# Kernel optimization log

Hardware: AMD Instinct MI355X
Metric: run time of the kernel (lower is better)

The kernel has to match this reference:

```python
import math
import jax, jax.numpy as jnp
import numpy as np

D = 128
R = 64
BETA = 1.0


def setup_inputs() -> dict:
    key = jax.random.key(0)
    k1, k2 = jax.random.split(key)
    X_tilde = jax.random.normal(k1, (8, 2048, D), dtype=jnp.float32)
    W = jax.random.normal(k2, (D, R), dtype=jnp.float32) / math.sqrt(R)
    return {"X_tilde": X_tilde, "W": W}


def reference(X_tilde, W):
    # S = W W^T / sqrt(d*r), shape (d, d)
    d, r = W.shape
    S = (W @ W.T) / math.sqrt(d * r)
    B, T, _ = X_tilde.shape
    # gram = X S X^T, shape (B, T, T)
    XS = jnp.einsum('btd,de->bte', X_tilde, S)
    gram = jnp.einsum('bte,bse->bts', XS, X_tilde)
    # trace-centering: subtract (tr(gram)/T) * I
    trace = jnp.einsum('btt->b', gram)  # (B,)
    eye = jnp.eye(T, dtype=X_tilde.dtype)
    centered = gram - (trace / T)[:, None, None] * eye[None, :, :]
    scores = centered / math.sqrt(d)  # normalize_sqrt_d=True
    A = jax.nn.softmax(BETA * scores, axis=-1)  # (B, T, T)
    Y_hat = jnp.einsum('bts,bsd->btd', A, X_tilde)
    return Y_hat
```

## Files before the change

kernel.cpp:

```cpp
#include <hip/hip_runtime.h>
#include <hip/hip_bf16.h>
#include <math.h>

#define D_DIM 128
#define R_DIM 64
#define T_DIM 2048
#define B_DIM 8
#define NS 4
#define SCHUNK (T_DIM / NS)
#define SBLK 32
#define NIT (SCHUNK / SBLK)
#define KE_CONST (0.08838834764831845f * 1.4426950408889634f)

typedef __attribute__((ext_vector_type(8))) short bf16x8;
typedef __attribute__((ext_vector_type(4))) short s16x4;
typedef __attribute__((ext_vector_type(4))) float f32x4;

__device__ inline unsigned short f2bf(float f) {
  union { float f; unsigned int u; } v; v.f = f;
  return (unsigned short)((v.u + 0x7FFFu + ((v.u >> 16) & 1u)) >> 16);
}
__device__ inline float bf2f(unsigned short u) {
  union { unsigned int u; float f; } v; v.u = ((unsigned int)u) << 16;
  return v.f;
}
__device__ inline unsigned int cvt_pk_bf16(float lo, float hi) {
  unsigned int r;
  asm("v_cvt_pk_bf16_f32 %0, %1, %2" : "=v"(r) : "v"(lo), "v"(hi));
  return r;
}

__device__ inline void async16(const short* l, const unsigned short* g) {
  __builtin_amdgcn_global_load_lds(
      (const __attribute__((address_space(1))) unsigned int*)g,
      (__attribute__((address_space(3))) unsigned int*)l, 16, 0, 0);
}

__global__ void k_s(const float* __restrict__ W, unsigned short* __restrict__ Sb) {
  int gid = blockIdx.x * 256 + threadIdx.x;
  int i = gid >> 7, j = gid & 127;
  const float* wi = W + i * R_DIM;
  const float* wj = W + j * R_DIM;
  float acc = 0.f;
#pragma unroll 8
  for (int r = 0; r < R_DIM; ++r) acc += wi[r] * wj[r];
  Sb[gid] = f2bf(acc * 0.011048543456039806f);
}

__global__ void __launch_bounds__(128) k_prep(
    const float* __restrict__ X, const unsigned short* __restrict__ Sb,
    unsigned short* __restrict__ Qb, unsigned short* __restrict__ Xb,
    unsigned short* __restrict__ Xt, float* __restrict__ part) {
  const int tid = threadIdx.x;
  const int w = tid >> 6, lane = tid & 63;
  const int g = lane >> 4, c = lane & 15;
  const int b = blockIdx.y;
  const int t0 = blockIdx.x * 32;
  const int tw = t0 + w * 16;

  __shared__ __align__(16) short xbT[D_DIM * 32];
  __shared__ float red[2];

  union FU { unsigned int wd[4]; bf16x8 v; };
  bf16x8 xf[4];
#pragma unroll
  for (int kc = 0; kc < 4; ++kc) {
    const float* xp = X + ((size_t)(b * T_DIM + tw + c)) * D_DIM + kc * 32 + g * 8;
    f32x4 a = *(const f32x4*)xp;
    f32x4 bb = *(const f32x4*)(xp + 4);
    FU f;
    f.wd[0] = cvt_pk_bf16(a[0], a[1]);
    f.wd[1] = cvt_pk_bf16(a[2], a[3]);
    f.wd[2] = cvt_pk_bf16(bb[0], bb[1]);
    f.wd[3] = cvt_pk_bf16(bb[2], bb[3]);
    xf[kc] = f.v;
    *(bf16x8*)(Xb + ((size_t)(b * T_DIM + tw + c)) * D_DIM + kc * 32 + g * 8) = f.v;
#pragma unroll
    for (int jw = 0; jw < 4; ++jw) {
      unsigned int wv = f.wd[jw];
      int e = kc * 32 + g * 8 + jw * 2;
      xbT[(e + 0) * 32 + w * 16 + c] = (short)wv;
      xbT[(e + 1) * 32 + w * 16 + c] = (short)(wv >> 16);
    }
  }

  f32x4 acc[8];
#pragma unroll
  for (int dc = 0; dc < 8; ++dc) acc[dc] = (f32x4){0.f, 0.f, 0.f, 0.f};
#pragma unroll
  for (int dc = 0; dc < 8; ++dc) {
    bf16x8 sf[4];
#pragma unroll
    for (int kc = 0; kc < 4; ++kc)
      sf[kc] = *(const bf16x8*)(Sb + (size_t)(dc * 16 + c) * D_DIM + kc * 32 + g * 8);
#pragma unroll
    for (int kc = 0; kc < 4; ++kc)
      acc[dc] = __builtin_amdgcn_mfma_f32_16x16x32_bf16(xf[kc], sf[kc], acc[dc], 0, 0, 0);
  }

  __syncthreads();

  float trp = 0.f;
#pragma unroll
  for (int dc = 0; dc < 8; ++dc)
#pragma unroll
    for (int r = 0; r < 4; ++r) {
      float q = acc[dc][r];
      float x = bf2f((unsigned short)xbT[(dc * 16 + c) * 32 + w * 16 + g * 4 + r]);
      trp += q * x;
      unsigned int pk = cvt_pk_bf16(q * KE_CONST, 0.f);
      Qb[((size_t)(b * T_DIM + tw + g * 4 + r)) * D_DIM + dc * 16 + c] = (unsigned short)pk;
    }

#pragma unroll
  for (int p = 0; p < 4; ++p) {
    int row = p * 32 + (tid >> 2);
    bf16x8 v = *(const bf16x8*)&xbT[row * 32 + (tid & 3) * 8];
    *(bf16x8*)(Xt + ((size_t)(b * D_DIM + row)) * T_DIM + t0 + (tid & 3) * 8) = v;
  }

  trp += __shfl_xor(trp, 1); trp += __shfl_xor(trp, 2);
  trp += __shfl_xor(trp, 4); trp += __shfl_xor(trp, 8);
  trp += __shfl_xor(trp, 16); trp += __shfl_xor(trp, 32);
  if (lane == 0) red[w] = trp;
  __syncthreads();
  if (tid == 0) part[b * 64 + blockIdx.x] = red[0] + red[1];
}

__global__ void __launch_bounds__(256, 2) k_attn(
    const unsigned short* __restrict__ Qb, const unsigned short* __restrict__ Xb,
    const unsigned short* __restrict__ Xt, const float* __restrict__ part,
    unsigned short* __restrict__ accp, float* __restrict__ rsp) {
  const int tid = threadIdx.x;
  const int wave = tid >> 6, lane = tid & 63;
  const int g = lane >> 4, c = lane & 15;
  const int lin = blockIdx.x;
  const int b = lin & 7;
  const int kk = lin >> 3;
  const int ns = kk & 3;
  const int t0w = (kk >> 2) * 128 + wave * 32;

  const unsigned short* Qbb = Qb + (size_t)b * T_DIM * D_DIM;
  const unsigned short* Xbb = Xb + (size_t)b * T_DIM * D_DIM;
  const unsigned short* Xtb = Xt + (size_t)b * D_DIM * T_DIM;

  float tv = part[b * 64 + lane];
  tv += __shfl_xor(tv, 1); tv += __shfl_xor(tv, 2);
  tv += __shfl_xor(tv, 4); tv += __shfl_xor(tv, 8);
  tv += __shfl_xor(tv, 16); tv += __shfl_xor(tv, 32);
  const float ctrK = tv * (1.0f / T_DIM) * KE_CONST;

  __shared__ __align__(16) short sKs[2][SBLK * D_DIM];
  __shared__ __align__(16) short sVs[2][D_DIM * SBLK];
  __shared__ __align__(16) short sPa[4][32 * 40];

  int oK[4], oV;
#pragma unroll
  for (int kc = 0; kc < 4; ++kc)
    oK[kc] = c * 128 + (((kc * 4 + g) ^ (c & 7)) * 8);
  oV = c * 32 + ((g ^ (c & 3)) * 8);
  const int oPr = (g ^ ((c >> 2) & 3)) * 8;

  bf16x8 qf[2][4];
#pragma unroll
  for (int tt = 0; tt < 2; ++tt)
#pragma unroll
    for (int kc = 0; kc < 4; ++kc)
      qf[tt][kc] = *(const bf16x8*)(Qbb + (size_t)(t0w + tt * 16 + c) * D_DIM + kc * 32 + g * 8);

  bf16x8 ones;
#pragma unroll
  for (int j = 0; j < 8; ++j) ones[j] = (short)0x3F80;

  f32x4 acc[2][8];
#pragma unroll
  for (int tt = 0; tt < 2; ++tt)
#pragma unroll
    for (int dt = 0; dt < 8; ++dt) acc[tt][dt] = (f32x4){0.f, 0.f, 0.f, 0.f};
  f32x4 accD[2] = {(f32x4){0.f, 0.f, 0.f, 0.f}, (f32x4){0.f, 0.f, 0.f, 0.f}};

  const int s_beg = ns * SCHUNK;

  auto stage = [&](int buf, int sb) {
#pragma unroll
    for (int q = 0; q < 2; ++q) {
      int j = wave * 128 + q * 64 + lane;
      int row = j >> 4, sc = j & 15;
      int lc = sc ^ (row & 7);
      async16(&sKs[buf][(wave * 128 + q * 64) * 8],
              Xbb + (size_t)(sb + row) * D_DIM + lc * 8);
    }
#pragma unroll
    for (int q = 0; q < 2; ++q) {
      int j = wave * 128 + q * 64 + lane;
      int row = j >> 2, sc = j & 3;
      int lc = sc ^ (row & 3);
      async16(&sVs[buf][(wave * 128 + q * 64) * 8],
              Xtb + (size_t)row * T_DIM + sb + lc * 8);
    }
  };

  stage(0, s_beg);
  __syncthreads();

  for (int it = 0; it < NIT; ++it) {
    const int buf = it & 1;
    const int sb = s_beg + it * SBLK;
    if (it < NIT - 1) stage(buf ^ 1, sb + SBLK);

    const short* kb = &sKs[buf][0];
    const short* vb = &sVs[buf][0];
    const bool isdiag = (sb == t0w);

#pragma unroll
    for (int st = 0; st < 2; ++st) {
      bf16x8 kf[4];
#pragma unroll
      for (int kc = 0; kc < 4; ++kc)
        kf[kc] = *(const bf16x8*)(kb + oK[kc] + st * 16 * 128);
      f32x4 sc0 = (f32x4){0.f, 0.f, 0.f, 0.f};
      f32x4 sc1 = (f32x4){0.f, 0.f, 0.f, 0.f};
#pragma unroll
      for (int kc = 0; kc < 4; ++kc) {
        sc0 = __builtin_amdgcn_mfma_f32_16x16x32_bf16(qf[0][kc], kf[kc], sc0, 0, 0, 0);
        sc1 = __builtin_amdgcn_mfma_f32_16x16x32_bf16(qf[1][kc], kf[kc], sc1, 0, 0, 0);
      }
      const int gp = ((st * 2 + (c >> 3)) ^ g) * 8 + (c & 7);
#pragma unroll
      for (int tt = 0; tt < 2; ++tt) {
        f32x4 sc = tt ? sc1 : sc0;
        float p[4];
#pragma unroll
        for (int r = 0; r < 4; ++r) {
          float v = sc[r];
          if (isdiag && (st * 16 + c) == (tt * 16 + g * 4 + r)) v -= ctrK;
          p[r] = exp2f(v);
        }
        unsigned int w01 = cvt_pk_bf16(p[0], p[1]);
        unsigned int w23 = cvt_pk_bf16(p[2], p[3]);
        short* pw = &sPa[wave][(tt * 16 + g * 4) * 40 + gp];
        pw[0 * 40] = (short)w01;
        pw[1 * 40] = (short)(w01 >> 16);
        pw[2 * 40] = (short)w23;
        pw[3 * 40] = (short)(w23 >> 16);
      }
    }

    bf16x8 pf[2];
#pragma unroll
    for (int tt = 0; tt < 2; ++tt)
      pf[tt] = *(const bf16x8*)&sPa[wave][(tt * 16 + c) * 40 + oPr];
    accD[0] = __builtin_amdgcn_mfma_f32_16x16x32_bf16(pf[0], ones, accD[0], 0, 0, 0);
    accD[1] = __builtin_amdgcn_mfma_f32_16x16x32_bf16(pf[1], ones, accD[1], 0, 0, 0);
#pragma unroll
    for (int dt = 0; dt < 8; ++dt) {
      bf16x8 vf = *(const bf16x8*)(vb + oV + dt * 16 * 32);
      acc[0][dt] = __builtin_amdgcn_mfma_f32_16x16x32_bf16(pf[0], vf, acc[0][dt], 0, 0, 0);
      acc[1][dt] = __builtin_amdgcn_mfma_f32_16x16x32_bf16(pf[1], vf, acc[1][dt], 0, 0, 0);
    }

    __syncthreads();
  }

  const size_t pbase = ((size_t)(b * NS + ns)) * T_DIM * D_DIM;
#pragma unroll
  for (int tt = 0; tt < 2; ++tt)
#pragma unroll
    for (int dt = 0; dt < 8; ++dt) {
      unsigned int w01 = cvt_pk_bf16(acc[tt][dt][0], acc[tt][dt][1]);
      unsigned int w23 = cvt_pk_bf16(acc[tt][dt][2], acc[tt][dt][3]);
      size_t a0 = pbase + (size_t)(t0w + tt * 16 + g * 4) * D_DIM + dt * 16 + c;
      accp[a0 + 0 * D_DIM] = (unsigned short)w01;
      accp[a0 + 1 * D_DIM] = (unsigned short)(w01 >> 16);
      accp[a0 + 2 * D_DIM] = (unsigned short)w23;
      accp[a0 + 3 * D_DIM] = (unsigned short)(w23 >> 16);
    }
  if (c == 0) {
#pragma unroll
    for (int tt = 0; tt < 2; ++tt)
#pragma unroll
      for (int r = 0; r < 4; ++r)
        rsp[(b * NS + ns) * T_DIM + t0w + tt * 16 + g * 4 + r] = accD[tt][r];
  }
}

__global__ void __launch_bounds__(256) k_comb(
    const unsigned short* __restrict__ accp, const float* __restrict__ rsp,
    float* __restrict__ out) {
  const int lin = blockIdx.x;
  const int b = lin & 7;
  const int kk = lin >> 3;
  int ib = kk * 1024 + threadIdx.x * 4;
  int d = ib & 127;
  int t = ib >> 7;
  float num0 = 0.f, num1 = 0.f, num2 = 0.f, num3 = 0.f, den = 0.f;
#pragma unroll
  for (int ns = 0; ns < NS; ++ns) {
    const unsigned short* p =
        accp + (((size_t)(b * NS + ns)) * T_DIM + t) * D_DIM + d;
    s16x4 v = *(const s16x4*)p;
    num0 += bf2f((unsigned short)v[0]);
    num1 += bf2f((unsigned short)v[1]);
    num2 += bf2f((unsigned short)v[2]);
    num3 += bf2f((unsigned short)v[3]);
    den += rsp[(b * NS + ns) * T_DIM + t];
  }
  float inv = 1.0f / den;
  f32x4 o = (f32x4){num0 * inv, num1 * inv, num2 * inv, num3 * inv};
  *(f32x4*)(out + ((size_t)b * T_DIM * D_DIM + ib)) = o;
}

extern "C" void kernel_launch(void* const* d_in, const int* in_sizes, int n_in,
                              void* d_out, int out_size, void* d_ws, size_t ws_size,
                              hipStream_t stream) {
  const float* X = (const float*)d_in[0];
  const float* W = (const float*)d_in[1];
  float* out = (float*)d_out;
  char* ws = (char*)d_ws;

  unsigned short* Sb = (unsigned short*)(ws);
  float* part        = (float*)(ws + 32768);
  unsigned short* Qb = (unsigned short*)(ws + 65536);
  unsigned short* Xb = (unsigned short*)(ws + 65536 + 4194304);
  unsigned short* Xt = (unsigned short*)(ws + 65536 + 2 * 4194304);
  unsigned short* accp = (unsigned short*)(ws + 65536 + 3 * 4194304);
  float* rsp         = (float*)(ws + 65536 + 3 * 4194304 + 16777216);

  k_s<<<64, 256, 0, stream>>>(W, Sb);
  k_prep<<<dim3(T_DIM / 32, B_DIM), 128, 0, stream>>>(X, Sb, Qb, Xb, Xt, part);
  k_attn<<<(T_DIM / 128) * NS * B_DIM, 256, 0, stream>>>(Qb, Xb, Xt, part, accp, rsp);
  k_comb<<<B_DIM * 256, 256, 0, stream>>>(accp, rsp, out);
}
```

Before: 53.84 us.

## Switch attention to 32x32x16 MFMA with register-resident P via permlane swap

Rewrites the attention kernel to compute transposed scores with 32x32x16 bf16 MFMAs and feed the exponentiated probabilities straight into the PV MFMA, using v_permlane32_swap to rearrange them in registers instead of going through shared memory. The LDS double-buffered async staging of K and V is removed, and each wave loads its K and V fragments directly from global memory. The row-sum is accumulated in fp32 registers rather than with an MFMA against a ones vector. This cuts LDS traffic and barriers, but every wave now redundantly reads K/V from global or L2 with no overlap of loads and compute, and the output stores become scattered 2-byte writes.

```diff
diff --git a/kernel.cpp b/kernel.cpp
--- a/kernel.cpp
+++ b/kernel.cpp
@@ -15,6 +15,7 @@
 typedef __attribute__((ext_vector_type(8))) short bf16x8;
 typedef __attribute__((ext_vector_type(4))) short s16x4;
 typedef __attribute__((ext_vector_type(4))) float f32x4;
+typedef __attribute__((ext_vector_type(16))) float f32x16;
 
 __device__ inline unsigned short f2bf(float f) {
   union { float f; unsigned int u; } v; v.f = f;
@@ -29,11 +30,8 @@
   asm("v_cvt_pk_bf16_f32 %0, %1, %2" : "=v"(r) : "v"(lo), "v"(hi));
   return r;
 }
-
-__device__ inline void async16(const short* l, const unsigned short* g) {
-  __builtin_amdgcn_global_load_lds(
-      (const __attribute__((address_space(1))) unsigned int*)g,
-      (__attribute__((address_space(3))) unsigned int*)l, 16, 0, 0);
+__device__ inline void permswap(unsigned int& a, unsigned int& b) {
+  asm("v_permlane32_swap_b32 %0, %1" : "+v"(a), "+v"(b));
 }
 
 __global__ void k_s(const float* __restrict__ W, unsigned short* __restrict__ Sb) {
@@ -133,7 +131,8 @@
     unsigned short* __restrict__ accp, float* __restrict__ rsp) {
   const int tid = threadIdx.x;
   const int wave = tid >> 6, lane = tid & 63;
-  const int g = lane >> 4, c = lane & 15;
+  const int tl = lane & 31;
+  const int h = lane >> 5;
   const int lin = blockIdx.x;
   const int b = lin & 7;
   const int kk = lin >> 3;
@@ -150,138 +149,83 @@
   tv += __shfl_xor(tv, 16); tv += __shfl_xor(tv, 32);
   const float ctrK = tv * (1.0f / T_DIM) * KE_CONST;
 
-  __shared__ __align__(16) short sKs[2][SBLK * D_DIM];
-  __shared__ __align__(16) short sVs[2][D_DIM * SBLK];
-  __shared__ __align__(16) short sPa[4][32 * 40];
-
-  int oK[4], oV;
-#pragma unroll
-  for (int kc = 0; kc < 4; ++kc)
-    oK[kc] = c * 128 + (((kc * 4 + g) ^ (c & 7)) * 8);
-  oV = c * 32 + ((g ^ (c & 3)) * 8);
-  const int oPr = (g ^ ((c >> 2) & 3)) * 8;
-
-  bf16x8 qf[2][4];
-#pragma unroll
-  for (int tt = 0; tt < 2; ++tt)
-#pragma unroll
-    for (int kc = 0; kc < 4; ++kc)
-      qf[tt][kc] = *(const bf16x8*)(Qbb + (size_t)(t0w + tt * 16 + c) * D_DIM + kc * 32 + g * 8);
-
-  bf16x8 ones;
-#pragma unroll
-  for (int j = 0; j < 8; ++j) ones[j] = (short)0x3F80;
-
-  f32x4 acc[2][8];
-#pragma unroll
-  for (int tt = 0; tt < 2; ++tt)
-#pragma unroll
-    for (int dt = 0; dt < 8; ++dt) acc[tt][dt] = (f32x4){0.f, 0.f, 0.f, 0.f};
-  f32x4 accD[2] = {(f32x4){0.f, 0.f, 0.f, 0.f}, (f32x4){0.f, 0.f, 0.f, 0.f}};
+  bf16x8 qf[8];
+#pragma unroll
+  for (int kc = 0; kc < 8; ++kc)
+    qf[kc] = *(const bf16x8*)(Qbb + (size_t)(t0w + tl) * D_DIM + kc * 16 + h * 8);
+
+  f32x16 acc[4];
+#pragma unroll
+  for (int dt = 0; dt < 4; ++dt)
+#pragma unroll
+    for (int r = 0; r < 16; ++r) acc[dt][r] = 0.f;
+  float denacc = 0.f;
 
   const int s_beg = ns * SCHUNK;
 
-  auto stage = [&](int buf, int sb) {
-#pragma unroll
-    for (int q = 0; q < 2; ++q) {
-      int j = wave * 128 + q * 64 + lane;
-      int row = j >> 4, sc = j & 15;
-      int lc = sc ^ (row & 7);
-      async16(&sKs[buf][(wave * 128 + q * 64) * 8],
-              Xbb + (size_t)(sb + row) * D_DIM + lc * 8);
-    }
-#pragma unroll
-    for (int q = 0; q < 2; ++q) {
-      int j = wave * 128 + q * 64 + lane;
-      int row = j >> 2, sc = j & 3;
-      int lc = sc ^ (row & 3);
-      async16(&sVs[buf][(wave * 128 + q * 64) * 8],
-              Xtb + (size_t)row * T_DIM + sb + lc * 8);
-    }
-  };
-
-  stage(0, s_beg);
-  __syncthreads();
-
   for (int it = 0; it < NIT; ++it) {
-    const int buf = it & 1;
     const int sb = s_beg + it * SBLK;
-    if (it < NIT - 1) stage(buf ^ 1, sb + SBLK);
-
-    const short* kb = &sKs[buf][0];
-    const short* vb = &sVs[buf][0];
-    const bool isdiag = (sb == t0w);
-
-#pragma unroll
-    for (int st = 0; st < 2; ++st) {
-      bf16x8 kf[4];
-#pragma unroll
-      for (int kc = 0; kc < 4; ++kc)
-        kf[kc] = *(const bf16x8*)(kb + oK[kc] + st * 16 * 128);
-      f32x4 sc0 = (f32x4){0.f, 0.f, 0.f, 0.f};
-      f32x4 sc1 = (f32x4){0.f, 0.f, 0.f, 0.f};
-#pragma unroll
-      for (int kc = 0; kc < 4; ++kc) {
-        sc0 = __builtin_amdgcn_mfma_f32_16x16x32_bf16(qf[0][kc], kf[kc], sc0, 0, 0, 0);
-        sc1 = __builtin_amdgcn_mfma_f32_16x16x32_bf16(qf[1][kc], kf[kc], sc1, 0, 0, 0);
+
+    bf16x8 kf[8];
+#pragma unroll
+    for (int kc = 0; kc < 8; ++kc)
+      kf[kc] = *(const bf16x8*)(Xbb + (size_t)(sb + tl) * D_DIM + kc * 16 + h * 8);
+    bf16x8 vf[4][2];
+#pragma unroll
+    for (int dt = 0; dt < 4; ++dt)
+#pragma unroll
+      for (int sck = 0; sck < 2; ++sck)
+        vf[dt][sck] = *(const bf16x8*)(Xtb + (size_t)(dt * 32 + tl) * T_DIM +
+                                        sb + sck * 16 + h * 8);
+
+    f32x16 sc;
+#pragma unroll
+    for (int r = 0; r < 16; ++r) sc[r] = 0.f;
+#pragma unroll
+    for (int kc = 0; kc < 8; ++kc)
+      sc = __builtin_amdgcn_mfma_f32_32x32x16_bf16(kf[kc], qf[kc], sc, 0, 0, 0);
+
+    const bool isd = (sb == t0w);
+
+#pragma unroll
+    for (int sck = 0; sck < 2; ++sck) {
+      float p[8];
+#pragma unroll
+      for (int q = 0; q < 8; ++q) {
+        int rowid = (q & 3) + 8 * (q >> 2) + 16 * sck + 4 * h;
+        float v = sc[sck * 8 + q];
+        if (isd && rowid == tl) v -= ctrK;
+        p[q] = exp2f(v);
+        denacc += p[q];
       }
-      const int gp = ((st * 2 + (c >> 3)) ^ g) * 8 + (c & 7);
-#pragma unroll
-      for (int tt = 0; tt < 2; ++tt) {
-        f32x4 sc = tt ? sc1 : sc0;
-        float p[4];
-#pragma unroll
-        for (int r = 0; r < 4; ++r) {
-          float v = sc[r];
-          if (isdiag && (st * 16 + c) == (tt * 16 + g * 4 + r)) v -= ctrK;
-          p[r] = exp2f(v);
-        }
-        unsigned int w01 = cvt_pk_bf16(p[0], p[1]);
-        unsigned int w23 = cvt_pk_bf16(p[2], p[3]);
-        short* pw = &sPa[wave][(tt * 16 + g * 4) * 40 + gp];
-        pw[0 * 40] = (short)w01;
-        pw[1 * 40] = (short)(w01 >> 16);
-        pw[2 * 40] = (short)w23;
-        pw[3 * 40] = (short)(w23 >> 16);
-      }
-    }
-
-    bf16x8 pf[2];
-#pragma unroll
-    for (int tt = 0; tt < 2; ++tt)
-      pf[tt] = *(const bf16x8*)&sPa[wave][(tt * 16 + c) * 40 + oPr];
-    accD[0] = __builtin_amdgcn_mfma_f32_16x16x32_bf16(pf[0], ones, accD[0], 0, 0, 0);
-    accD[1] = __builtin_amdgcn_mfma_f32_16x16x32_bf16(pf[1], ones, accD[1], 0, 0, 0);
-#pragma unroll
-    for (int dt = 0; dt < 8; ++dt) {
-      bf16x8 vf = *(const bf16x8*)(vb + oV + dt * 16 * 32);
-      acc[0][dt] = __builtin_amdgcn_mfma_f32_16x16x32_bf16(pf[0], vf, acc[0][dt], 0, 0, 0);
-      acc[1][dt] = __builtin_amdgcn_mfma_f32_16x16x32_bf16(pf[1], vf, acc[1][dt], 0, 0, 0);
-    }
-
-    __syncthreads();
-  }
+      unsigned int W0 = cvt_pk_bf16(p[0], p[1]);
+      unsigned int W1 = cvt_pk_bf16(p[2], p[3]);
+      unsigned int W2 = cvt_pk_bf16(p[4], p[5]);
+      unsigned int W3 = cvt_pk_bf16(p[6], p[7]);
+      permswap(W0, W2);
+      permswap(W1, W3);
+      union PU { unsigned int wd[4]; bf16x8 v; } pu;
+      pu.wd[0] = W0; pu.wd[1] = W1; pu.wd[2] = W2; pu.wd[3] = W3;
+#pragma unroll
+      for (int dt = 0; dt < 4; ++dt)
+        acc[dt] = __builtin_amdgcn_mfma_f32_32x32x16_bf16(pu.v, vf[dt][sck],
+                                                          acc[dt], 0, 0, 0);
+    }
+  }
+
+  float den = denacc + __shfl_xor(denacc, 32);
+  if (lane < 32)
+    rsp[(b * NS + ns) * T_DIM + t0w + lane] = den;
 
   const size_t pbase = ((size_t)(b * NS + ns)) * T_DIM * D_DIM;
 #pragma unroll
-  for (int tt = 0; tt < 2; ++tt)
-#pragma unroll
-    for (int dt = 0; dt < 8; ++dt) {
-      unsigned int w01 = cvt_pk_bf16(acc[tt][dt][0], acc[tt][dt][1]);
-      unsigned int w23 = cvt_pk_bf16(acc[tt][dt][2], acc[tt][dt][3]);
-      size_t a0 = pbase + (size_t)(t0w + tt * 16 + g * 4) * D_DIM + dt * 16 + c;
-      accp[a0 + 0 * D_DIM] = (unsigned short)w01;
-      accp[a0 + 1 * D_DIM] = (unsigned short)(w01 >> 16);
-      accp[a0 + 2 * D_DIM] = (unsigned short)w23;
-      accp[a0 + 3 * D_DIM] = (unsigned short)(w23 >> 16);
-    }
-  if (c == 0) {
-#pragma unroll
-    for (int tt = 0; tt < 2; ++tt)
-#pragma unroll
-      for (int r = 0; r < 4; ++r)
-        rsp[(b * NS + ns) * T_DIM + t0w + tt * 16 + g * 4 + r] = accD[tt][r];
-  }
+  for (int dt = 0; dt < 4; ++dt)
+#pragma unroll
+    for (int r = 0; r < 16; ++r) {
+      int rowid = (r & 3) + 8 * (r >> 2) + 4 * h;
+      accp[pbase + (size_t)(t0w + rowid) * D_DIM + dt * 32 + tl] =
+          (unsigned short)cvt_pk_bf16(acc[dt][r], 0.f);
+    }
 }
 
 __global__ void __launch_bounds__(256) k_comb(
```

Result: slower. 91.80 us (+70.5%).
